# Kernel optimization log

Measured on AMD Instinct MI355X. Metric: run time of the kernel, lower is better.

The kernel has to match this reference:

```python
import jax, jax.numpy as jnp
import numpy as np

VOCAB, EMBED, FILT, LABELS = 30522, 256, 256, 50
B, S = 32, 4096

def setup_inputs() -> dict:
    key = jax.random.key(0)
    k0, k1, k2, k3, k4 = jax.random.split(key, 5)
    return {
        "input_ids": jax.random.randint(k0, (B, S), 0, VOCAB),
        "emb_table": jax.random.normal(k1, (VOCAB, EMBED), dtype=jnp.float32) * 0.02,
        "conv_w": jax.random.normal(k2, (FILT, EMBED, 4), dtype=jnp.float32) * 0.05,  # (out_ch, in_ch, k)
        "conv_b": jnp.zeros((FILT,), dtype=jnp.float32),
        "U_w": jax.random.normal(k3, (LABELS, FILT), dtype=jnp.float32) * 0.05,  # torch Linear weight layout
        "final_w": jax.random.normal(k4, (LABELS, FILT), dtype=jnp.float32) * 0.05,
        "final_b": jnp.zeros((LABELS,), dtype=jnp.float32),
    }

def reference(input_ids, emb_table, conv_w, conv_b, U_w, final_w, final_b):
    # Embedding lookup: (B, S, E) -> NCH layout (B, E, S)
    x = jnp.take(emb_table, input_ids, axis=0).transpose(0, 2, 1)
    # Conv1d(kernel=4, padding=2): output length S+1
    h = jax.lax.conv_general_dilated(
        x, conv_w, window_strides=(1,), padding=[(2, 2)],
        dimension_numbers=("NCH", "OIH", "NCH"))
    H = jnp.tanh(h + conv_b[None, :, None]).transpose(0, 2, 1)  # (B, S+1, F)
    # Per-label attention: softmax over the sequence dimension
    scores = jnp.einsum("bsf,lf->bsl", H, U_w)          # (B, S+1, L)
    alpha = jax.nn.softmax(scores, axis=1)
    m = jnp.einsum("bsl,bsf->blf", alpha, H)             # (B, L, F)
    logits = jnp.sum(m * final_w[None], axis=2) + final_b  # (B, L)
    return logits
```

## Files before the change

kernel.cpp:

```cpp
#include <hip/hip_runtime.h>
#include <hip/hip_bf16.h>
#include <stdint.h>

#define BDIM 32
#define SDIM 4096
#define SP1  4097
#define EDIM 256
#define FDIM 256
#define LDIM 50
#define TTILE 96
#define NT    43

typedef __attribute__((ext_vector_type(8))) short bf16x8v;
typedef __attribute__((ext_vector_type(4))) float f32x4;

__device__ __forceinline__ unsigned short f2bf(float f) {
    union { float f; uint32_t u; } v; v.f = f;
    uint32_t u = v.u;
    uint32_t r = (u + 0x7fffu + ((u >> 16) & 1u)) >> 16;
    return (unsigned short)r;
}

__device__ __forceinline__ float tanh_fast(float x) {
    float e = __expf(2.0f * x);
    float r = __builtin_amdgcn_rcpf(e + 1.0f);
    return fmaf(-2.0f, r, 1.0f);
}

__device__ __forceinline__ uint32_t pack_bf2(float lo, float hi) {
    union { __hip_bfloat162 v; uint32_t u; } cv;
    cv.v = __halves2bfloat162(__float2bfloat16(lo), __float2bfloat16(hi));
    return cv.u;
}

__device__ __forceinline__ void load_lds16(const void* g, uint32_t* l) {
    __builtin_amdgcn_global_load_lds(
        (const __attribute__((address_space(1))) uint32_t*)g,
        (__attribute__((address_space(3))) uint32_t*)l, 16, 0, 0);
}

__global__ void prep_misc(const float* __restrict__ conv_w,
                          const float* __restrict__ U_w, const float* __restrict__ final_w,
                          unsigned short* __restrict__ Wb2, unsigned short* __restrict__ W2k,
                          uint32_t* __restrict__ zp) {
    int o = blockIdx.x * 256 + threadIdx.x;
    {
        int kk = o & 1023, f = o >> 10;
        int e = kk & 255, k = kk >> 8;
        int g = kk >> 5, h4 = (kk >> 3) & 3, j = kk & 7;
        Wb2[((size_t)(g * 4 + h4) * 256 + f) * 8 + j] = f2bf(conv_w[f * 1024 + e * 4 + k]);
    }
    if (o < 32768) {
        int j = o & 7, c = (o >> 3) & 127, g = o >> 10;
        int k = g * 8 + j, l = c & 63;
        float v = 0.f;
        if (l < LDIM) v = (c < 64) ? U_w[l * FDIM + k] : final_w[l * FDIM + k];
        W2k[o] = f2bf(v);
    }
    if (o < 128) zp[o] = 0;
}

__global__ void prep_embb(const float* __restrict__ emb, unsigned short* __restrict__ embb) {
    size_t o = ((size_t)blockIdx.x * 256 + threadIdx.x) * 8;
    if (o >= (size_t)30522 * 256) return;
    float4 v0 = *(const float4*)(emb + o);
    float4 v1 = *(const float4*)(emb + o + 4);
    union { unsigned short u[8]; uint4 q; } pk;
    pk.u[0] = f2bf(v0.x); pk.u[1] = f2bf(v0.y); pk.u[2] = f2bf(v0.z); pk.u[3] = f2bf(v0.w);
    pk.u[4] = f2bf(v1.x); pk.u[5] = f2bf(v1.y); pk.u[6] = f2bf(v1.z); pk.u[7] = f2bf(v1.w);
    *(uint4*)(embb + o) = pk.q;
}

__global__ __launch_bounds__(256, 2) void fused_kernel(
    const int* __restrict__ ids, const unsigned short* __restrict__ embb,
    const unsigned short* __restrict__ Wb2, const float* __restrict__ conv_b,
    const unsigned short* __restrict__ W2k, const uint32_t* __restrict__ zp,
    float* __restrict__ part)
{
    __shared__ uint32_t xs[100 * 128];

    const int tid  = threadIdx.x;
    const int lane = tid & 63;
    const int wid  = tid >> 6;
    const int b    = blockIdx.y;
    const int tile = blockIdx.x;
    const int t0   = tile * TTILE;
    const int l15  = lane & 15;
    const int hi4  = lane >> 4;
    const int q    = lane & 31;
    const int half = lane >> 5;

    {
        int nid[13];
        #pragma unroll
        for (int j = 0; j < 13; ++j) {
            int r0 = wid * 2 + j * 8;
            int r  = r0 + half;
            int p  = t0 - 2 + r;
            nid[j] = -1;
            if (r0 < 100 && r < 99 && (unsigned)p < SDIM)
                nid[j] = ids[b * SDIM + p];
        }
        const unsigned short* zs = (const unsigned short*)zp + q * 8;
        const uint32_t soff = ((uint32_t)(q * 16) ^ ((uint32_t)((wid * 2 + half) & 7) << 4)) >> 1;
        #pragma unroll
        for (int j = 0; j < 13; ++j) {
            int r0 = wid * 2 + j * 8;
            if (r0 >= 100) continue;
            int r = r0 + half;
            const unsigned short* s = (nid[j] >= 0)
                ? embb + (size_t)nid[j] * EDIM + (((uint32_t)(q * 16) ^ ((uint32_t)(r & 7) << 4)) >> 1)
                : zs;
            load_lds16(s, &xs[r0 * 128]);
        }
        (void)soff;
    }
    __syncthreads();

    const int fbase = wid * 64;
    const unsigned short* afbase = Wb2 + (size_t)(hi4 * 256 + fbase + l15) * 8;

    f32x4 acc[4][6];
    #pragma unroll
    for (int a = 0; a < 4; ++a)
        #pragma unroll
        for (int n = 0; n < 6; ++n) acc[a][n] = (f32x4){0.f, 0.f, 0.f, 0.f};

    bf16x8v afc[4];
    #pragma unroll
    for (int a = 0; a < 4; ++a) afc[a] = *(const bf16x8v*)(afbase + a * 128);

    #pragma unroll 1
    for (int k = 0; k < 4; ++k) {
        uint32_t bb[6];
        #pragma unroll
        for (int n = 0; n < 6; ++n) {
            int r = n * 16 + l15 + k;
            bb[n] = (uint32_t)(r * 512) ^ (uint32_t)(hi4 * 16) ^ (uint32_t)((r & 7) << 4);
        }
        const unsigned short* afg = afbase + (size_t)k * 65536;
        #pragma unroll
        for (int es = 0; es < 8; ++es) {
            const unsigned short* nxt = (es < 7)
                ? (afg + (size_t)(es + 1) * 8192)
                : (afbase + (size_t)((k + 1) & 3) * 65536);
            bf16x8v afn[4];
            #pragma unroll
            for (int a = 0; a < 4; ++a) afn[a] = *(const bf16x8v*)(nxt + a * 128);

            bf16x8v bfr[6];
            #pragma unroll
            for (int n = 0; n < 6; ++n)
                bfr[n] = *(const bf16x8v*)((const char*)xs + (bb[n] ^ (uint32_t)(es * 64)));

            __builtin_amdgcn_s_setprio(1);
            #pragma unroll
            for (int a = 0; a < 4; ++a)
                #pragma unroll
                for (int n = 0; n < 6; ++n)
                    acc[a][n] = __builtin_amdgcn_mfma_f32_16x16x32_bf16(afc[a], bfr[n], acc[a][n], 0, 0, 0);
            __builtin_amdgcn_s_setprio(0);

            #pragma unroll
            for (int a = 0; a < 4; ++a) afc[a] = afn[a];
        }
    }
    __syncthreads();

    float4 cb[4];
    #pragma unroll
    for (int a = 0; a < 4; ++a)
        cb[a] = *(const float4*)(conv_b + fbase + a * 16 + hi4 * 4);
    #pragma unroll
    for (int n = 0; n < 6; ++n) {
        int tl = n * 16 + l15;
        uint32_t hb = (uint32_t)(tl * 512) ^ (uint32_t)(hi4 * 8)
                    ^ (uint32_t)(fbase * 2) ^ (uint32_t)((tl & 7) << 4);
        #pragma unroll
        for (int a = 0; a < 4; ++a) {
            f32x4 d = acc[a][n];
            uint2 pk;
            pk.x = pack_bf2(tanh_fast(d[0] + cb[a].x), tanh_fast(d[1] + cb[a].y));
            pk.y = pack_bf2(tanh_fast(d[2] + cb[a].z), tanh_fast(d[3] + cb[a].w));
            *(uint2*)((char*)xs + (hb ^ (uint32_t)(a * 32))) = pk;
        }
    }
    __syncthreads();

    const int cbase = wid * 16;
    f32x4 p2[6][2];
    #pragma unroll
    for (int m = 0; m < 6; ++m) { p2[m][0] = (f32x4){0,0,0,0}; p2[m][1] = (f32x4){0,0,0,0}; }

    uint32_t pb[6];
    #pragma unroll
    for (int m = 0; m < 6; ++m) {
        int sl = m * 16 + l15;
        pb[m] = (uint32_t)(sl * 512) ^ (uint32_t)(hi4 * 16) ^ (uint32_t)((sl & 7) << 4);
    }
    const unsigned short* wp0 = W2k + (size_t)(hi4 * 128 + cbase + l15) * 8;

    #pragma unroll
    for (int step = 0; step < 8; ++step) {
        bf16x8v ha[6], w2[2];
        #pragma unroll
        for (int m = 0; m < 6; ++m)
            ha[m] = *(const bf16x8v*)((const char*)xs + (pb[m] ^ (uint32_t)(step * 64)));
        w2[0] = *(const bf16x8v*)(wp0 + step * 4096);
        w2[1] = *(const bf16x8v*)(wp0 + 512 + step * 4096);
        __builtin_amdgcn_s_setprio(1);
        #pragma unroll
        for (int m = 0; m < 6; ++m) {
            p2[m][0] = __builtin_amdgcn_mfma_f32_16x16x32_bf16(ha[m], w2[0], p2[m][0], 0, 0, 0);
            p2[m][1] = __builtin_amdgcn_mfma_f32_16x16x32_bf16(ha[m], w2[1], p2[m][1], 0, 0, 0);
        }
        __builtin_amdgcn_s_setprio(0);
    }

    float mx = -1e30f;
    #pragma unroll
    for (int m = 0; m < 6; ++m)
        #pragma unroll
        for (int i = 0; i < 4; ++i) {
            int s = t0 + m * 16 + hi4 * 4 + i;
            if (s <= SDIM) mx = fmaxf(mx, p2[m][0][i]);
        }
    float se = 0.f, st = 0.f;
    #pragma unroll
    for (int m = 0; m < 6; ++m)
        #pragma unroll
        for (int i = 0; i < 4; ++i) {
            int s = t0 + m * 16 + hi4 * 4 + i;
            if (s <= SDIM) {
                float e = __expf(p2[m][0][i] - mx);
                se += e;
                st += e * p2[m][1][i];
            }
        }
    #pragma unroll
    for (int d = 16; d <= 32; d <<= 1) {
        float mo  = __shfl_xor(mx, d);
        float seo = __shfl_xor(se, d);
        float sto = __shfl_xor(st, d);
        float M  = fmaxf(mx, mo);
        float w0 = __expf(mx - M), w1 = __expf(mo - M);
        se = se * w0 + seo * w1;
        st = st * w0 + sto * w1;
        mx = M;
    }
    if (lane < 16) {
        int l = cbase + l15;
        if (l < LDIM) {
            size_t o = (((size_t)b * NT + tile) * LDIM + l) * 3;
            part[o] = mx; part[o + 1] = se; part[o + 2] = st;
        }
    }
}

__global__ void final_kernel(const float* __restrict__ part, const float* __restrict__ final_b,
                             float* __restrict__ out)
{
    int b = blockIdx.x, l = threadIdx.x;
    if (l >= LDIM) return;
    float mx = -1e30f, se = 0.f, st = 0.f;
    for (int c = 0; c < NT; ++c) {
        size_t o = (((size_t)b * NT + c) * LDIM + l) * 3;
        float mo = part[o], seo = part[o + 1], sto = part[o + 2];
        float M  = fmaxf(mx, mo);
        float w0 = __expf(mx - M), w1 = __expf(mo - M);
        se = se * w0 + seo * w1;
        st = st * w0 + sto * w1;
        mx = M;
    }
    out[b * LDIM + l] = st / se + final_b[l];
}

extern "C" void kernel_launch(void* const* d_in, const int* in_sizes, int n_in,
                              void* d_out, int out_size, void* d_ws, size_t ws_size,
                              hipStream_t stream)
{
    const int*   ids     = (const int*)d_in[0];
    const float* emb     = (const float*)d_in[1];
    const float* conv_w  = (const float*)d_in[2];
    const float* conv_b  = (const float*)d_in[3];
    const float* U_w     = (const float*)d_in[4];
    const float* final_w = (const float*)d_in[5];
    const float* final_b = (const float*)d_in[6];

    char* ws = (char*)d_ws;
    size_t offE  = 0;
    size_t szE   = (size_t)30522 * 256 * 2;
    size_t offWb = offE + szE;
    size_t szWb  = 256 * 1024 * 2;
    size_t offW2 = offWb + szWb;
    size_t szW2  = 32768 * 2;
    size_t offZ  = offW2 + szW2;
    size_t szZ   = 512;
    size_t offP  = offZ + szZ;

    unsigned short* embb = (unsigned short*)(ws + offE);
    unsigned short* Wb2  = (unsigned short*)(ws + offWb);
    unsigned short* W2k  = (unsigned short*)(ws + offW2);
    uint32_t*       zp   = (uint32_t*)(ws + offZ);
    float*          prt  = (float*)(ws + offP);

    prep_misc<<<1024, 256, 0, stream>>>(conv_w, U_w, final_w, Wb2, W2k, zp);
    prep_embb<<<3816, 256, 0, stream>>>(emb, embb);
    fused_kernel<<<dim3(NT, BDIM), 256, 0, stream>>>(ids, embb, Wb2, conv_b, W2k, zp, prt);
    final_kernel<<<BDIM, 64, 0, stream>>>(prt, final_b, (float*)d_out);
}
```

Measured before the change: 105.6 us.

## Use 128-wide time tiles, peel last position into final kernel, merge prep kernels

Raises the time tile from 96 to 128 so the sequence divides evenly into 32 tiles, removing per-element bounds checks and the partial tail tile. The extra output position is computed in fp32 inside the final reduction kernel and seeded into the online softmax. The two preprocessing kernels are merged into one launch. Larger tiles increase LDS use and accumulator registers, and may affect occupancy.

```diff
diff --git a/kernel.cpp b/kernel.cpp
--- a/kernel.cpp
+++ b/kernel.cpp
@@ -8,8 +8,8 @@
 #define EDIM 256
 #define FDIM 256
 #define LDIM 50
-#define TTILE 96
-#define NT    43
+#define TTILE 128
+#define NT    32
 
 typedef __attribute__((ext_vector_type(8))) short bf16x8v;
 typedef __attribute__((ext_vector_type(4))) float f32x4;
@@ -39,12 +39,22 @@
         (__attribute__((address_space(3))) uint32_t*)l, 16, 0, 0);
 }
 
-__global__ void prep_misc(const float* __restrict__ conv_w,
-                          const float* __restrict__ U_w, const float* __restrict__ final_w,
-                          unsigned short* __restrict__ Wb2, unsigned short* __restrict__ W2k,
-                          uint32_t* __restrict__ zp) {
+__global__ void prep_all(const float* __restrict__ emb, const float* __restrict__ conv_w,
+                         const float* __restrict__ U_w, const float* __restrict__ final_w,
+                         unsigned short* __restrict__ embb, unsigned short* __restrict__ Wb2,
+                         unsigned short* __restrict__ W2k, uint32_t* __restrict__ zp)
+{
     int o = blockIdx.x * 256 + threadIdx.x;
-    {
+    size_t eo = (size_t)o * 8;
+    if (eo < (size_t)30522 * 256) {
+        float4 v0 = *(const float4*)(emb + eo);
+        float4 v1 = *(const float4*)(emb + eo + 4);
+        union { unsigned short u[8]; uint4 q; } pk;
+        pk.u[0] = f2bf(v0.x); pk.u[1] = f2bf(v0.y); pk.u[2] = f2bf(v0.z); pk.u[3] = f2bf(v0.w);
+        pk.u[4] = f2bf(v1.x); pk.u[5] = f2bf(v1.y); pk.u[6] = f2bf(v1.z); pk.u[7] = f2bf(v1.w);
+        *(uint4*)(embb + eo) = pk.q;
+    }
+    if (o < 262144) {
         int kk = o & 1023, f = o >> 10;
         int e = kk & 255, k = kk >> 8;
         int g = kk >> 5, h4 = (kk >> 3) & 3, j = kk & 7;
@@ -60,24 +70,13 @@
     if (o < 128) zp[o] = 0;
 }
 
-__global__ void prep_embb(const float* __restrict__ emb, unsigned short* __restrict__ embb) {
-    size_t o = ((size_t)blockIdx.x * 256 + threadIdx.x) * 8;
-    if (o >= (size_t)30522 * 256) return;
-    float4 v0 = *(const float4*)(emb + o);
-    float4 v1 = *(const float4*)(emb + o + 4);
-    union { unsigned short u[8]; uint4 q; } pk;
-    pk.u[0] = f2bf(v0.x); pk.u[1] = f2bf(v0.y); pk.u[2] = f2bf(v0.z); pk.u[3] = f2bf(v0.w);
-    pk.u[4] = f2bf(v1.x); pk.u[5] = f2bf(v1.y); pk.u[6] = f2bf(v1.z); pk.u[7] = f2bf(v1.w);
-    *(uint4*)(embb + o) = pk.q;
-}
-
 __global__ __launch_bounds__(256, 2) void fused_kernel(
     const int* __restrict__ ids, const unsigned short* __restrict__ embb,
     const unsigned short* __restrict__ Wb2, const float* __restrict__ conv_b,
     const unsigned short* __restrict__ W2k, const uint32_t* __restrict__ zp,
     float* __restrict__ part)
 {
-    __shared__ uint32_t xs[100 * 128];
+    __shared__ uint32_t xs[132 * 128];
 
     const int tid  = threadIdx.x;
     const int lane = tid & 63;
@@ -91,40 +90,38 @@
     const int half = lane >> 5;
 
     {
-        int nid[13];
-        #pragma unroll
-        for (int j = 0; j < 13; ++j) {
+        int nid[17];
+        #pragma unroll
+        for (int j = 0; j < 17; ++j) {
             int r0 = wid * 2 + j * 8;
             int r  = r0 + half;
             int p  = t0 - 2 + r;
             nid[j] = -1;
-            if (r0 < 100 && r < 99 && (unsigned)p < SDIM)
+            if (r0 < 131 && r < 131 && (unsigned)p < SDIM)
                 nid[j] = ids[b * SDIM + p];
         }
         const unsigned short* zs = (const unsigned short*)zp + q * 8;
-        const uint32_t soff = ((uint32_t)(q * 16) ^ ((uint32_t)((wid * 2 + half) & 7) << 4)) >> 1;
-        #pragma unroll
-        for (int j = 0; j < 13; ++j) {
+        #pragma unroll
+        for (int j = 0; j < 17; ++j) {
             int r0 = wid * 2 + j * 8;
-            if (r0 >= 100) continue;
+            if (r0 >= 131) continue;
             int r = r0 + half;
             const unsigned short* s = (nid[j] >= 0)
                 ? embb + (size_t)nid[j] * EDIM + (((uint32_t)(q * 16) ^ ((uint32_t)(r & 7) << 4)) >> 1)
                 : zs;
             load_lds16(s, &xs[r0 * 128]);
         }
-        (void)soff;
     }
     __syncthreads();
 
     const int fbase = wid * 64;
     const unsigned short* afbase = Wb2 + (size_t)(hi4 * 256 + fbase + l15) * 8;
 
-    f32x4 acc[4][6];
+    f32x4 acc[4][8];
     #pragma unroll
     for (int a = 0; a < 4; ++a)
         #pragma unroll
-        for (int n = 0; n < 6; ++n) acc[a][n] = (f32x4){0.f, 0.f, 0.f, 0.f};
+        for (int n = 0; n < 8; ++n) acc[a][n] = (f32x4){0.f, 0.f, 0.f, 0.f};
 
     bf16x8v afc[4];
     #pragma unroll
@@ -132,9 +129,9 @@
 
     #pragma unroll 1
     for (int k = 0; k < 4; ++k) {
-        uint32_t bb[6];
-        #pragma unroll
-        for (int n = 0; n < 6; ++n) {
+        uint32_t bb[8];
+        #pragma unroll
+        for (int n = 0; n < 8; ++n) {
             int r = n * 16 + l15 + k;
             bb[n] = (uint32_t)(r * 512) ^ (uint32_t)(hi4 * 16) ^ (uint32_t)((r & 7) << 4);
         }
@@ -148,16 +145,16 @@
             #pragma unroll
             for (int a = 0; a < 4; ++a) afn[a] = *(const bf16x8v*)(nxt + a * 128);
 
-            bf16x8v bfr[6];
+            bf16x8v bfr[8];
             #pragma unroll
-            for (int n = 0; n < 6; ++n)
+            for (int n = 0; n < 8; ++n)
                 bfr[n] = *(const bf16x8v*)((const char*)xs + (bb[n] ^ (uint32_t)(es * 64)));
 
             __builtin_amdgcn_s_setprio(1);
             #pragma unroll
             for (int a = 0; a < 4; ++a)
                 #pragma unroll
-                for (int n = 0; n < 6; ++n)
+                for (int n = 0; n < 8; ++n)
                     acc[a][n] = __builtin_amdgcn_mfma_f32_16x16x32_bf16(afc[a], bfr[n], acc[a][n], 0, 0, 0);
             __builtin_amdgcn_s_setprio(0);
 
@@ -172,7 +169,7 @@
     for (int a = 0; a < 4; ++a)
         cb[a] = *(const float4*)(conv_b + fbase + a * 16 + hi4 * 4);
     #pragma unroll
-    for (int n = 0; n < 6; ++n) {
+    for (int n = 0; n < 8; ++n) {
         int tl = n * 16 + l15;
         uint32_t hb = (uint32_t)(tl * 512) ^ (uint32_t)(hi4 * 8)
                     ^ (uint32_t)(fbase * 2) ^ (uint32_t)((tl & 7) << 4);
@@ -188,13 +185,13 @@
     __syncthreads();
 
     const int cbase = wid * 16;
-    f32x4 p2[6][2];
-    #pragma unroll
-    for (int m = 0; m < 6; ++m) { p2[m][0] = (f32x4){0,0,0,0}; p2[m][1] = (f32x4){0,0,0,0}; }
-
-    uint32_t pb[6];
-    #pragma unroll
-    for (int m = 0; m < 6; ++m) {
+    f32x4 p2[8][2];
+    #pragma unroll
+    for (int m = 0; m < 8; ++m) { p2[m][0] = (f32x4){0,0,0,0}; p2[m][1] = (f32x4){0,0,0,0}; }
+
+    uint32_t pb[8];
+    #pragma unroll
+    for (int m = 0; m < 8; ++m) {
         int sl = m * 16 + l15;
         pb[m] = (uint32_t)(sl * 512) ^ (uint32_t)(hi4 * 16) ^ (uint32_t)((sl & 7) << 4);
     }
@@ -202,15 +199,15 @@
 
     #pragma unroll
     for (int step = 0; step < 8; ++step) {
-        bf16x8v ha[6], w2[2];
-        #pragma unroll
-        for (int m = 0; m < 6; ++m)
+        bf16x8v ha[8], w2[2];
+        #pragma unroll
+        for (int m = 0; m < 8; ++m)
             ha[m] = *(const bf16x8v*)((const char*)xs + (pb[m] ^ (uint32_t)(step * 64)));
         w2[0] = *(const bf16x8v*)(wp0 + step * 4096);
         w2[1] = *(const bf16x8v*)(wp0 + 512 + step * 4096);
         __builtin_amdgcn_s_setprio(1);
         #pragma unroll
-        for (int m = 0; m < 6; ++m) {
+        for (int m = 0; m < 8; ++m) {
             p2[m][0] = __builtin_amdgcn_mfma_f32_16x16x32_bf16(ha[m], w2[0], p2[m][0], 0, 0, 0);
             p2[m][1] = __builtin_amdgcn_mfma_f32_16x16x32_bf16(ha[m], w2[1], p2[m][1], 0, 0, 0);
         }
@@ -219,23 +216,18 @@
 
     float mx = -1e30f;
     #pragma unroll
-    for (int m = 0; m < 6; ++m)
+    for (int m = 0; m < 8; ++m)
+        #pragma unroll
+        for (int i = 0; i < 4; ++i)
+            mx = fmaxf(mx, p2[m][0][i]);
+    float se = 0.f, st = 0.f;
+    #pragma unroll
+    for (int m = 0; m < 8; ++m)
         #pragma unroll
         for (int i = 0; i < 4; ++i) {
-            int s = t0 + m * 16 + hi4 * 4 + i;
-            if (s <= SDIM) mx = fmaxf(mx, p2[m][0][i]);
-        }
-    float se = 0.f, st = 0.f;
-    #pragma unroll
-    for (int m = 0; m < 6; ++m)
-        #pragma unroll
-        for (int i = 0; i < 4; ++i) {
-            int s = t0 + m * 16 + hi4 * 4 + i;
-            if (s <= SDIM) {
-                float e = __expf(p2[m][0][i] - mx);
-                se += e;
-                st += e * p2[m][1][i];
-            }
+            float e = __expf(p2[m][0][i] - mx);
+            se += e;
+            st += e * p2[m][1][i];
         }
     #pragma unroll
     for (int d = 16; d <= 32; d <<= 1) {
@@ -257,22 +249,49 @@
     }
 }
 
-__global__ void final_kernel(const float* __restrict__ part, const float* __restrict__ final_b,
+__global__ void final_kernel(const int* __restrict__ ids, const float* __restrict__ emb,
+                             const float* __restrict__ conv_w, const float* __restrict__ conv_b,
+                             const float* __restrict__ U_w, const float* __restrict__ final_w,
+                             const float* __restrict__ part, const float* __restrict__ final_b,
                              float* __restrict__ out)
 {
-    int b = blockIdx.x, l = threadIdx.x;
-    if (l >= LDIM) return;
-    float mx = -1e30f, se = 0.f, st = 0.f;
-    for (int c = 0; c < NT; ++c) {
-        size_t o = (((size_t)b * NT + c) * LDIM + l) * 3;
-        float mo = part[o], seo = part[o + 1], sto = part[o + 2];
-        float M  = fmaxf(mx, mo);
-        float w0 = __expf(mx - M), w1 = __expf(mo - M);
-        se = se * w0 + seo * w1;
-        st = st * w0 + sto * w1;
-        mx = M;
-    }
-    out[b * LDIM + l] = st / se + final_b[l];
+    __shared__ float hsh[FDIM];
+    int b = blockIdx.x, t = threadIdx.x;
+
+    {
+        int id0 = ids[b * SDIM + 4094];
+        int id1 = ids[b * SDIM + 4095];
+        const float* e0 = emb + (size_t)id0 * EDIM;
+        const float* e1 = emb + (size_t)id1 * EDIM;
+        const float* wf = conv_w + (size_t)t * 1024;
+        float a = conv_b[t];
+        #pragma unroll 4
+        for (int e = 0; e < 256; ++e)
+            a += wf[e * 4] * e0[e] + wf[e * 4 + 1] * e1[e];
+        hsh[t] = tanhf(a);
+    }
+    __syncthreads();
+
+    if (t < LDIM) {
+        float sc = 0.f, tv = 0.f;
+        #pragma unroll 4
+        for (int f = 0; f < 256; ++f) {
+            float h = hsh[f];
+            sc += h * U_w[t * FDIM + f];
+            tv += h * final_w[t * FDIM + f];
+        }
+        float mx = sc, se = 1.0f, st = tv;
+        for (int c = 0; c < NT; ++c) {
+            size_t o = (((size_t)b * NT + c) * LDIM + t) * 3;
+            float mo = part[o], seo = part[o + 1], sto = part[o + 2];
+            float M  = fmaxf(mx, mo);
+            float w0 = __expf(mx - M), w1 = __expf(mo - M);
+            se = se * w0 + seo * w1;
+            st = st * w0 + sto * w1;
+            mx = M;
+        }
+        out[b * LDIM + t] = st / se + final_b[t];
+    }
 }
 
 extern "C" void kernel_launch(void* const* d_in, const int* in_sizes, int n_in,
@@ -304,8 +323,8 @@
     uint32_t*       zp   = (uint32_t*)(ws + offZ);
     float*          prt  = (float*)(ws + offP);
 
-    prep_misc<<<1024, 256, 0, stream>>>(conv_w, U_w, final_w, Wb2, W2k, zp);
-    prep_embb<<<3816, 256, 0, stream>>>(emb, embb);
+    prep_all<<<3816, 256, 0, stream>>>(emb, conv_w, U_w, final_w, embb, Wb2, W2k, zp);
     fused_kernel<<<dim3(NT, BDIM), 256, 0, stream>>>(ids, embb, Wb2, conv_b, W2k, zp, prt);
-    final_kernel<<<BDIM, 64, 0, stream>>>(prt, final_b, (float*)d_out);
-}
+    final_kernel<<<BDIM, 256, 0, stream>>>(ids, emb, conv_w, conv_b, U_w, final_w,
+                                           prt, final_b, (float*)d_out);
+}
```

New measurement: 122.7 us. +16.1%, slower.
